# Performance work log

Measured on AMD Instinct MI355X. Metric: run time of the kernel, lower is better.

Reference implementation:

```python
import jax, jax.numpy as jnp
import numpy as np

N_NODES = 50000
N_EDGES = 800000
D = 128
BN_EPS = 1e-5


def setup_inputs() -> dict:
    key = jax.random.key(0)
    ks = jax.random.split(key, 8)
    scale = 1.0 / np.sqrt(D)
    return {
        "nfeat": jax.random.normal(ks[0], (N_NODES, D), dtype=jnp.float32),
        "efeat": jax.random.normal(ks[1], (N_EDGES, D), dtype=jnp.float32),
        "src": jax.random.randint(ks[2], (N_EDGES,), 0, N_NODES, dtype=jnp.int32),
        "dst": jax.random.randint(ks[3], (N_EDGES,), 0, N_NODES, dtype=jnp.int32),
        "W1": jax.random.normal(ks[4], (D, D), dtype=jnp.float32) * scale,
        "b1": jnp.zeros((D,), dtype=jnp.float32),
        "gamma": jnp.ones((D,), dtype=jnp.float32),
        "beta": jnp.zeros((D,), dtype=jnp.float32),
        "W2": jax.random.normal(ks[5], (D, D), dtype=jnp.float32) * scale,
        "b2": jnp.zeros((D,), dtype=jnp.float32),
        "We": jax.random.normal(ks[6], (D, D), dtype=jnp.float32) * scale,
        "be": jnp.zeros((D,), dtype=jnp.float32),
    }


def reference(nfeat, efeat, src, dst, W1, b1, gamma, beta, W2, b2, We, be):
    n = nfeat.shape[0]
    # GINConv, sum aggregator, eps=0: h = (1+eps)*x + sum_{j in N(i)} x_j
    agg = jax.ops.segment_sum(nfeat[src], dst, num_segments=n)  # [N, D]
    h = nfeat + agg
    # apply_func: Linear -> BatchNorm1d (training-mode batch stats) -> ReLU -> Linear
    h = h @ W1 + b1
    mu = jnp.mean(h, axis=0)
    var = jnp.mean(jnp.square(h - mu), axis=0)  # biased variance, as BatchNorm uses
    h = gamma * (h - mu) * jax.lax.rsqrt(var + BN_EPS) + beta
    h = jax.nn.relu(h)
    h = h @ W2 + b2
    # edge branch: linear on edge feats, scatter-sum to destination nodes, residual add
    e = efeat @ We + be                                          # [E, D]
    h_e = jax.ops.segment_sum(e, dst, num_segments=n)            # [N, D]
    return h + h_e
```

## Files before the change

### kernel.cpp

```cpp
#include <hip/hip_runtime.h>

#define D 128
#define TR 64
#define BK 32

static __device__ __forceinline__ float4 f4add(float4 a, float4 b) {
    return make_float4(a.x + b.x, a.y + b.y, a.z + b.z, a.w + b.w);
}


__global__ void k_hist(const int* __restrict__ dst, int* __restrict__ cnt, int E) {
    const int e = blockIdx.x * 256 + threadIdx.x;
    if (e < E) atomicAdd(&cnt[dst[e]], 1);
}

__global__ __launch_bounds__(256) void k_scan1(const int* __restrict__ cnt,
                                               int* __restrict__ row_ptr,
                                               int* __restrict__ bsum, int N) {
    __shared__ int sh[256];
    const int t = threadIdx.x;
    const int base = blockIdx.x * 1024 + t * 4;
    int4 v = make_int4(0, 0, 0, 0);
    if (base + 3 < N) v = *(const int4*)(cnt + base);
    else {
        if (base     < N) v.x = cnt[base];
        if (base + 1 < N) v.y = cnt[base + 1];
        if (base + 2 < N) v.z = cnt[base + 2];
        if (base + 3 < N) v.w = cnt[base + 3];
    }
    const int s = v.x + v.y + v.z + v.w;
    sh[t] = s;
    __syncthreads();
    for (int off = 1; off < 256; off <<= 1) {
        int tmp = (t >= off) ? sh[t - off] : 0;
        __syncthreads();
        sh[t] += tmp;
        __syncthreads();
    }
    const int p = sh[t] - s;
    if (base     < N) row_ptr[base]     = p;
    if (base + 1 < N) row_ptr[base + 1] = p + v.x;
    if (base + 2 < N) row_ptr[base + 2] = p + v.x + v.y;
    if (base + 3 < N) row_ptr[base + 3] = p + v.x + v.y + v.z;
    if (t == 255) bsum[blockIdx.x] = sh[255];
}

__global__ __launch_bounds__(256) void k_scan2(int* __restrict__ bsum, int nb) {
    __shared__ int sh[256];
    const int t = threadIdx.x;
    const int v = (t < nb) ? bsum[t] : 0;
    sh[t] = v;
    __syncthreads();
    for (int off = 1; off < 256; off <<= 1) {
        int tmp = (t >= off) ? sh[t - off] : 0;
        __syncthreads();
        sh[t] += tmp;
        __syncthreads();
    }
    if (t < nb) bsum[t] = sh[t] - v;
}

__global__ __launch_bounds__(256) void k_scan3(int* __restrict__ row_ptr,
                                               int* __restrict__ cursor,
                                               const int* __restrict__ bsum,
                                               int N, int E) {
    const int t = threadIdx.x;
    const int base = blockIdx.x * 1024 + t * 4;
    const int off = bsum[blockIdx.x];
    #pragma unroll
    for (int j = 0; j < 4; ++j) {
        const int i = base + j;
        if (i < N) {
            const int r = row_ptr[i] + off;
            row_ptr[i] = r;
            cursor[i] = r;
        }
    }
    if (blockIdx.x == 0 && t == 0) row_ptr[N] = E;
}

__global__ void k_scatter(const int* __restrict__ src, const int* __restrict__ dst,
                          int* __restrict__ cursor,
                          int* __restrict__ eidx, int* __restrict__ esrc, int E) {
    const int e = blockIdx.x * 256 + threadIdx.x;
    if (e < E) {
        const int d = dst[e];
        const int p = atomicAdd(&cursor[d], 1);
        eidx[p] = e;
        esrc[p] = src[e];
    }
}

__global__ __launch_bounds__(256) void k_gather(const float* __restrict__ nfeat,
                                                const float* __restrict__ efeat,
                                                const int* __restrict__ row_ptr,
                                                const int* __restrict__ eidx,
                                                const int* __restrict__ esrc,
                                                float* __restrict__ agg_n,
                                                float* __restrict__ agg_e,
                                                int N) {
    const int t = threadIdx.x;
    const int lane = t & 63;
    const int node = blockIdx.x * 4 + (t >> 6);
    if (node >= N) return;
    const float2* nf2 = (const float2*)nfeat;
    const float2* ef2 = (const float2*)efeat;
    const int start = row_ptr[node];
    const int end = row_ptr[node + 1];
    float2 an = make_float2(0.f, 0.f);
    float2 ae = make_float2(0.f, 0.f);
    int i = start;
    for (; i + 1 < end; i += 2) {
        const int e0 = eidx[i],     s0 = esrc[i];
        const int e1 = eidx[i + 1], s1 = esrc[i + 1];
        const float2 ev0 = ef2[(size_t)e0 * 64 + lane];
        const float2 nv0 = nf2[(size_t)s0 * 64 + lane];
        const float2 ev1 = ef2[(size_t)e1 * 64 + lane];
        const float2 nv1 = nf2[(size_t)s1 * 64 + lane];
        ae.x += ev0.x + ev1.x; ae.y += ev0.y + ev1.y;
        an.x += nv0.x + nv1.x; an.y += nv0.y + nv1.y;
    }
    if (i < end) {
        const int e0 = eidx[i], s0 = esrc[i];
        const float2 ev0 = ef2[(size_t)e0 * 64 + lane];
        const float2 nv0 = nf2[(size_t)s0 * 64 + lane];
        ae.x += ev0.x; ae.y += ev0.y;
        an.x += nv0.x; an.y += nv0.y;
    }
    ((float2*)agg_n)[(size_t)node * 64 + lane] = an;
    ((float2*)agg_e)[(size_t)node * 64 + lane] = ae;
}

#define FMA_ROW(i, xv)                                                         \
    acc[i][0] += xv * w0.x; acc[i][1] += xv * w0.y;                            \
    acc[i][2] += xv * w0.z; acc[i][3] += xv * w0.w;                            \
    acc[i][4] += xv * w1.x; acc[i][5] += xv * w1.y;                            \
    acc[i][6] += xv * w1.z; acc[i][7] += xv * w1.w;

__global__ __launch_bounds__(256) void k_h1(const float* __restrict__ nfeat,
                                            const float* __restrict__ agg_n,
                                            const float* __restrict__ W1,
                                            const float* __restrict__ b1,
                                            float* __restrict__ h1,
                                            float* __restrict__ stats,
                                            int N) {
    __shared__ float xs[TR * 132];
    __shared__ float wsh[BK * 128];
    const int t = threadIdx.x;
    const int row0 = blockIdx.x * TR;

    for (int i = t; i < TR * 32; i += 256) {
        const int r = i >> 5, c4 = i & 31;
        const int row = row0 + r;
        float4 v = make_float4(0.f, 0.f, 0.f, 0.f);
        if (row < N) {
            const float4 a = *(const float4*)(nfeat + row * D + c4 * 4);
            const float4 g = *(const float4*)(agg_n + row * D + c4 * 4);
            v = f4add(a, g);
        }
        *(float4*)(xs + r * 132 + c4 * 4) = v;
    }

    float acc[4][8];
    #pragma unroll
    for (int i = 0; i < 4; ++i)
        #pragma unroll
        for (int j = 0; j < 8; ++j) acc[i][j] = 0.f;

    const int rg = (t >> 4) * 4;
    const int c  = t & 15;

    for (int kc = 0; kc < D; kc += BK) {
        __syncthreads();
        #pragma unroll
        for (int i = 0; i < 4; ++i) {
            const int slot = i * 256 + t;
            const int k = slot >> 5, ch = slot & 31;
            *(float4*)(wsh + k * 128 + ch * 4) =
                *(const float4*)(W1 + (kc + k) * D + ch * 4);
        }
        __syncthreads();
        #pragma unroll 8
        for (int k = 0; k < BK; ++k) {
            const float4 w0 = *(const float4*)(wsh + k * 128 + c * 4);
            const float4 w1 = *(const float4*)(wsh + k * 128 + 64 + c * 4);
            const float x0 = xs[(rg + 0) * 132 + kc + k];
            const float x1 = xs[(rg + 1) * 132 + kc + k];
            const float x2 = xs[(rg + 2) * 132 + kc + k];
            const float x3 = xs[(rg + 3) * 132 + kc + k];
            FMA_ROW(0, x0)
            FMA_ROW(1, x1)
            FMA_ROW(2, x2)
            FMA_ROW(3, x3)
        }
    }

    const float4 bb0 = *(const float4*)(b1 + c * 4);
    const float4 bb1 = *(const float4*)(b1 + 64 + c * 4);
    float cs[8], cq[8];
    #pragma unroll
    for (int j = 0; j < 8; ++j) { cs[j] = 0.f; cq[j] = 0.f; }

    #pragma unroll
    for (int i = 0; i < 4; ++i) {
        const int row = row0 + rg + i;
        if (row < N) {
            float h[8];
            h[0] = acc[i][0] + bb0.x; h[1] = acc[i][1] + bb0.y;
            h[2] = acc[i][2] + bb0.z; h[3] = acc[i][3] + bb0.w;
            h[4] = acc[i][4] + bb1.x; h[5] = acc[i][5] + bb1.y;
            h[6] = acc[i][6] + bb1.z; h[7] = acc[i][7] + bb1.w;
            *(float4*)(h1 + row * D + c * 4)      = make_float4(h[0], h[1], h[2], h[3]);
            *(float4*)(h1 + row * D + 64 + c * 4) = make_float4(h[4], h[5], h[6], h[7]);
            #pragma unroll
            for (int j = 0; j < 8; ++j) { cs[j] += h[j]; cq[j] += h[j] * h[j]; }
        }
    }

    __syncthreads();
    float* red = wsh;
    const int g = t >> 4;
    #pragma unroll
    for (int j = 0; j < 4; ++j) {
        red[g * 256 +       4 * c + j] = cs[j];
        red[g * 256 +  64 + 4 * c + j] = cs[4 + j];
        red[g * 256 + 128 + 4 * c + j] = cq[j];
        red[g * 256 + 192 + 4 * c + j] = cq[4 + j];
    }
    __syncthreads();
    float v = 0.f;
    #pragma unroll
    for (int g2 = 0; g2 < 16; ++g2) v += red[g2 * 256 + t];
    atomicAdd(stats + t, v);
}

__global__ void k_bn_finalize(float* __restrict__ stats,
                              const float* __restrict__ gamma,
                              const float* __restrict__ beta,
                              int N) {
    const int c = threadIdx.x;
    const float invN = 1.0f / (float)N;
    const float sum = stats[c];
    const float sq  = stats[D + c];
    const float mu  = sum * invN;
    const float var = sq * invN - mu * mu;
    const float sc  = gamma[c] * rsqrtf(var + 1e-5f);
    const float sh  = beta[c] - mu * sc;
    stats[c]     = sc;
    stats[D + c] = sh;
}

__global__ __launch_bounds__(256) void k_out(const float* __restrict__ h1,
                                             const float* __restrict__ agg_e,
                                             const float* __restrict__ stats,
                                             const float* __restrict__ W2,
                                             const float* __restrict__ b2,
                                             const float* __restrict__ We,
                                             const float* __restrict__ be,
                                             const int* __restrict__ row_ptr,
                                             float* __restrict__ out,
                                             int N) {
    __shared__ float xs[TR * 132];
    __shared__ float wsh[BK * 128];
    const int t = threadIdx.x;
    const int row0 = blockIdx.x * TR;
    const int rg = (t >> 4) * 4;
    const int c  = t & 15;

    float acc[4][8];
    #pragma unroll
    for (int i = 0; i < 4; ++i)
        #pragma unroll
        for (int j = 0; j < 8; ++j) acc[i][j] = 0.f;

    for (int i = t; i < TR * 32; i += 256) {
        const int r = i >> 5, c4 = i & 31;
        const int row = row0 + r;
        float4 v = make_float4(0.f, 0.f, 0.f, 0.f);
        if (row < N) {
            const float4 h  = *(const float4*)(h1 + row * D + c4 * 4);
            const float4 sc = *(const float4*)(stats + c4 * 4);
            const float4 sh = *(const float4*)(stats + 128 + c4 * 4);
            v.x = fmaxf(h.x * sc.x + sh.x, 0.f);
            v.y = fmaxf(h.y * sc.y + sh.y, 0.f);
            v.z = fmaxf(h.z * sc.z + sh.z, 0.f);
            v.w = fmaxf(h.w * sc.w + sh.w, 0.f);
        }
        *(float4*)(xs + r * 132 + c4 * 4) = v;
    }
    for (int kc = 0; kc < D; kc += BK) {
        __syncthreads();
        #pragma unroll
        for (int i = 0; i < 4; ++i) {
            const int slot = i * 256 + t;
            const int k = slot >> 5, ch = slot & 31;
            *(float4*)(wsh + k * 128 + ch * 4) =
                *(const float4*)(W2 + (kc + k) * D + ch * 4);
        }
        __syncthreads();
        #pragma unroll 8
        for (int k = 0; k < BK; ++k) {
            const float4 w0 = *(const float4*)(wsh + k * 128 + c * 4);
            const float4 w1 = *(const float4*)(wsh + k * 128 + 64 + c * 4);
            const float x0 = xs[(rg + 0) * 132 + kc + k];
            const float x1 = xs[(rg + 1) * 132 + kc + k];
            const float x2 = xs[(rg + 2) * 132 + kc + k];
            const float x3 = xs[(rg + 3) * 132 + kc + k];
            FMA_ROW(0, x0)
            FMA_ROW(1, x1)
            FMA_ROW(2, x2)
            FMA_ROW(3, x3)
        }
    }
    __syncthreads();

    for (int i = t; i < TR * 32; i += 256) {
        const int r = i >> 5, c4 = i & 31;
        const int row = row0 + r;
        float4 v = make_float4(0.f, 0.f, 0.f, 0.f);
        if (row < N) v = *(const float4*)(agg_e + row * D + c4 * 4);
        *(float4*)(xs + r * 132 + c4 * 4) = v;
    }
    for (int kc = 0; kc < D; kc += BK) {
        __syncthreads();
        #pragma unroll
        for (int i = 0; i < 4; ++i) {
            const int slot = i * 256 + t;
            const int k = slot >> 5, ch = slot & 31;
            *(float4*)(wsh + k * 128 + ch * 4) =
                *(const float4*)(We + (kc + k) * D + ch * 4);
        }
        __syncthreads();
        #pragma unroll 8
        for (int k = 0; k < BK; ++k) {
            const float4 w0 = *(const float4*)(wsh + k * 128 + c * 4);
            const float4 w1 = *(const float4*)(wsh + k * 128 + 64 + c * 4);
            const float x0 = xs[(rg + 0) * 132 + kc + k];
            const float x1 = xs[(rg + 1) * 132 + kc + k];
            const float x2 = xs[(rg + 2) * 132 + kc + k];
            const float x3 = xs[(rg + 3) * 132 + kc + k];
            FMA_ROW(0, x0)
            FMA_ROW(1, x1)
            FMA_ROW(2, x2)
            FMA_ROW(3, x3)
        }
    }

    const float4 b20 = *(const float4*)(b2 + c * 4);
    const float4 b21 = *(const float4*)(b2 + 64 + c * 4);
    const float4 be0 = *(const float4*)(be + c * 4);
    const float4 be1 = *(const float4*)(be + 64 + c * 4);
    #pragma unroll
    for (int i = 0; i < 4; ++i) {
        const int row = row0 + rg + i;
        if (row < N) {
            const float dg = (float)(row_ptr[row + 1] - row_ptr[row]);
            const float4 o0 = make_float4(acc[i][0] + b20.x + dg * be0.x,
                                          acc[i][1] + b20.y + dg * be0.y,
                                          acc[i][2] + b20.z + dg * be0.z,
                                          acc[i][3] + b20.w + dg * be0.w);
            const float4 o1 = make_float4(acc[i][4] + b21.x + dg * be1.x,
                                          acc[i][5] + b21.y + dg * be1.y,
                                          acc[i][6] + b21.z + dg * be1.z,
                                          acc[i][7] + b21.w + dg * be1.w);
            *(float4*)(out + row * D + c * 4)      = o0;
            *(float4*)(out + row * D + 64 + c * 4) = o1;
        }
    }
}

extern "C" void kernel_launch(void* const* d_in, const int* in_sizes, int n_in,
                              void* d_out, int out_size, void* d_ws, size_t ws_size,
                              hipStream_t stream) {
    const float* nfeat = (const float*)d_in[0];
    const float* efeat = (const float*)d_in[1];
    const int*   src   = (const int*)d_in[2];
    const int*   dst   = (const int*)d_in[3];
    const float* W1    = (const float*)d_in[4];
    const float* b1    = (const float*)d_in[5];
    const float* gamma = (const float*)d_in[6];
    const float* beta  = (const float*)d_in[7];
    const float* W2    = (const float*)d_in[8];
    const float* b2    = (const float*)d_in[9];
    const float* We    = (const float*)d_in[10];
    const float* be    = (const float*)d_in[11];
    float* out = (float*)d_out;

    const int N = in_sizes[0] / D;
    const int E = in_sizes[2];

    float* ws      = (float*)d_ws;
    float* agg_n   = ws;
    float* h1      = agg_n;
    float* agg_e   = ws + (size_t)N * D;
    float* stats   = ws + (size_t)2 * N * D;
    int*   row_ptr = (int*)(stats + 256);
    int*   cursor  = row_ptr + (N + 16);
    int*   cnt     = cursor + (N + 16);
    int*   bsum    = cnt + (N + 16);
    int*   eidx    = bsum + 64;
    int*   esrc    = eidx + E;

    hipMemsetAsync(cnt, 0, (size_t)N * sizeof(int), stream);
    hipMemsetAsync(stats, 0, 256 * sizeof(float), stream);

    const int ebl = (E + 255) / 256;
    const int scb = (N + 1023) / 1024;

    k_hist<<<ebl, 256, 0, stream>>>(dst, cnt, E);
    k_scan1<<<scb, 256, 0, stream>>>(cnt, row_ptr, bsum, N);
    k_scan2<<<1, 256, 0, stream>>>(bsum, scb);
    k_scan3<<<scb, 256, 0, stream>>>(row_ptr, cursor, bsum, N, E);
    k_scatter<<<ebl, 256, 0, stream>>>(src, dst, cursor, eidx, esrc, E);

    k_gather<<<(N + 3) / 4, 256, 0, stream>>>(nfeat, efeat, row_ptr, eidx, esrc,
                                              agg_n, agg_e, N);

    const int nb = (N + TR - 1) / TR;
    k_h1<<<nb, 256, 0, stream>>>(nfeat, agg_n, W1, b1, h1, stats, N);
    k_bn_finalize<<<1, 128, 0, stream>>>(stats, gamma, beta, N);
    k_out<<<nb, 256, 0, stream>>>(h1, agg_e, stats, W2, b2, We, be, row_ptr, out, N);
}
```

Baseline: 345.8 us.

## Pack edge pairs, split wave across edges, fuse self-add into gather

The two memsets become a single zeroing kernel. The histogram and scatter kernels now handle four edges per thread through int4 loads of dst/src, and the scatter writes one interleaved int2 (edge index, source) per slot instead of two separate arrays. The gather kernel uses float4 loads with each half-wave taking alternate edges and combines the halves with a cross-lane shuffle; it also adds the node's own features, so k_h1 reads one buffer instead of two. These changes target launch overhead, index-load count and redundant feature reads, at the cost of extra shuffles and idle half-waves on low-degree nodes.

```diff
diff --git a/kernel.cpp b/kernel.cpp
--- a/kernel.cpp
+++ b/kernel.cpp
@@ -8,10 +8,23 @@
     return make_float4(a.x + b.x, a.y + b.y, a.z + b.z, a.w + b.w);
 }
 
+__global__ void k_zero(int* __restrict__ cnt, float* __restrict__ stats, int N) {
+    const int i = blockIdx.x * 256 + threadIdx.x;
+    if (i < N) cnt[i] = 0;
+    if (i < 256) stats[i] = 0.f;
+}
 
 __global__ void k_hist(const int* __restrict__ dst, int* __restrict__ cnt, int E) {
-    const int e = blockIdx.x * 256 + threadIdx.x;
-    if (e < E) atomicAdd(&cnt[dst[e]], 1);
+    const int base = (blockIdx.x * 256 + threadIdx.x) * 4;
+    if (base + 3 < E) {
+        const int4 d4 = *(const int4*)(dst + base);
+        atomicAdd(&cnt[d4.x], 1);
+        atomicAdd(&cnt[d4.y], 1);
+        atomicAdd(&cnt[d4.z], 1);
+        atomicAdd(&cnt[d4.w], 1);
+    } else {
+        for (int e = base; e < E; ++e) atomicAdd(&cnt[dst[e]], 1);
+    }
 }
 
 __global__ __launch_bounds__(256) void k_scan1(const int* __restrict__ cnt,
@@ -81,54 +94,65 @@
 
 __global__ void k_scatter(const int* __restrict__ src, const int* __restrict__ dst,
                           int* __restrict__ cursor,
-                          int* __restrict__ eidx, int* __restrict__ esrc, int E) {
-    const int e = blockIdx.x * 256 + threadIdx.x;
-    if (e < E) {
-        const int d = dst[e];
-        const int p = atomicAdd(&cursor[d], 1);
-        eidx[p] = e;
-        esrc[p] = src[e];
+                          int2* __restrict__ epair, int E) {
+    const int base = (blockIdx.x * 256 + threadIdx.x) * 4;
+    if (base + 3 < E) {
+        const int4 d4 = *(const int4*)(dst + base);
+        const int4 s4 = *(const int4*)(src + base);
+        int p;
+        p = atomicAdd(&cursor[d4.x], 1); epair[p] = make_int2(base + 0, s4.x);
+        p = atomicAdd(&cursor[d4.y], 1); epair[p] = make_int2(base + 1, s4.y);
+        p = atomicAdd(&cursor[d4.z], 1); epair[p] = make_int2(base + 2, s4.z);
+        p = atomicAdd(&cursor[d4.w], 1); epair[p] = make_int2(base + 3, s4.w);
+    } else {
+        for (int e = base; e < E; ++e) {
+            const int p = atomicAdd(&cursor[dst[e]], 1);
+            epair[p] = make_int2(e, src[e]);
+        }
     }
 }
 
 __global__ __launch_bounds__(256) void k_gather(const float* __restrict__ nfeat,
                                                 const float* __restrict__ efeat,
                                                 const int* __restrict__ row_ptr,
-                                                const int* __restrict__ eidx,
-                                                const int* __restrict__ esrc,
-                                                float* __restrict__ agg_n,
+                                                const int2* __restrict__ epair,
+                                                float* __restrict__ xbuf,
                                                 float* __restrict__ agg_e,
                                                 int N) {
     const int t = threadIdx.x;
     const int lane = t & 63;
+    const int h = lane >> 5;
+    const int c = lane & 31;
     const int node = blockIdx.x * 4 + (t >> 6);
     if (node >= N) return;
-    const float2* nf2 = (const float2*)nfeat;
-    const float2* ef2 = (const float2*)efeat;
+
     const int start = row_ptr[node];
-    const int end = row_ptr[node + 1];
-    float2 an = make_float2(0.f, 0.f);
-    float2 ae = make_float2(0.f, 0.f);
-    int i = start;
-    for (; i + 1 < end; i += 2) {
-        const int e0 = eidx[i],     s0 = esrc[i];
-        const int e1 = eidx[i + 1], s1 = esrc[i + 1];
-        const float2 ev0 = ef2[(size_t)e0 * 64 + lane];
-        const float2 nv0 = nf2[(size_t)s0 * 64 + lane];
-        const float2 ev1 = ef2[(size_t)e1 * 64 + lane];
-        const float2 nv1 = nf2[(size_t)s1 * 64 + lane];
-        ae.x += ev0.x + ev1.x; ae.y += ev0.y + ev1.y;
-        an.x += nv0.x + nv1.x; an.y += nv0.y + nv1.y;
-    }
-    if (i < end) {
-        const int e0 = eidx[i], s0 = esrc[i];
-        const float2 ev0 = ef2[(size_t)e0 * 64 + lane];
-        const float2 nv0 = nf2[(size_t)s0 * 64 + lane];
-        ae.x += ev0.x; ae.y += ev0.y;
-        an.x += nv0.x; an.y += nv0.y;
-    }
-    ((float2*)agg_n)[(size_t)node * 64 + lane] = an;
-    ((float2*)agg_e)[(size_t)node * 64 + lane] = ae;
+    const int end   = row_ptr[node + 1];
+
+    float4 an = make_float4(0.f, 0.f, 0.f, 0.f);
+    float4 ae = make_float4(0.f, 0.f, 0.f, 0.f);
+    for (int e = start + h; e < end; e += 2) {
+        const int2 p = epair[e];
+        const float4 ev = *(const float4*)(efeat + (size_t)p.x * D + c * 4);
+        const float4 nv = *(const float4*)(nfeat + (size_t)p.y * D + c * 4);
+        ae = f4add(ae, ev);
+        an = f4add(an, nv);
+    }
+    float4 an_t, ae_t;
+    an_t.x = an.x + __shfl_xor(an.x, 32);
+    an_t.y = an.y + __shfl_xor(an.y, 32);
+    an_t.z = an.z + __shfl_xor(an.z, 32);
+    an_t.w = an.w + __shfl_xor(an.w, 32);
+    ae_t.x = ae.x + __shfl_xor(ae.x, 32);
+    ae_t.y = ae.y + __shfl_xor(ae.y, 32);
+    ae_t.z = ae.z + __shfl_xor(ae.z, 32);
+    ae_t.w = ae.w + __shfl_xor(ae.w, 32);
+
+    if (h == 0) {
+        const float4 self = *(const float4*)(nfeat + (size_t)node * D + c * 4);
+        *(float4*)(xbuf  + (size_t)node * D + c * 4) = f4add(self, an_t);
+        *(float4*)(agg_e + (size_t)node * D + c * 4) = ae_t;
+    }
 }
 
 #define FMA_ROW(i, xv)                                                         \
@@ -137,8 +161,7 @@
     acc[i][4] += xv * w1.x; acc[i][5] += xv * w1.y;                            \
     acc[i][6] += xv * w1.z; acc[i][7] += xv * w1.w;
 
-__global__ __launch_bounds__(256) void k_h1(const float* __restrict__ nfeat,
-                                            const float* __restrict__ agg_n,
+__global__ __launch_bounds__(256) void k_h1(const float* __restrict__ xbuf,
                                             const float* __restrict__ W1,
                                             const float* __restrict__ b1,
                                             float* __restrict__ h1,
@@ -153,11 +176,7 @@
         const int r = i >> 5, c4 = i & 31;
         const int row = row0 + r;
         float4 v = make_float4(0.f, 0.f, 0.f, 0.f);
-        if (row < N) {
-            const float4 a = *(const float4*)(nfeat + row * D + c4 * 4);
-            const float4 g = *(const float4*)(agg_n + row * D + c4 * 4);
-            v = f4add(a, g);
-        }
+        if (row < N) v = *(const float4*)(xbuf + (size_t)row * D + c4 * 4);
         *(float4*)(xs + r * 132 + c4 * 4) = v;
     }
 
@@ -210,8 +229,8 @@
             h[2] = acc[i][2] + bb0.z; h[3] = acc[i][3] + bb0.w;
             h[4] = acc[i][4] + bb1.x; h[5] = acc[i][5] + bb1.y;
             h[6] = acc[i][6] + bb1.z; h[7] = acc[i][7] + bb1.w;
-            *(float4*)(h1 + row * D + c * 4)      = make_float4(h[0], h[1], h[2], h[3]);
-            *(float4*)(h1 + row * D + 64 + c * 4) = make_float4(h[4], h[5], h[6], h[7]);
+            *(float4*)(h1 + (size_t)row * D + c * 4)      = make_float4(h[0], h[1], h[2], h[3]);
+            *(float4*)(h1 + (size_t)row * D + 64 + c * 4) = make_float4(h[4], h[5], h[6], h[7]);
             #pragma unroll
             for (int j = 0; j < 8; ++j) { cs[j] += h[j]; cq[j] += h[j] * h[j]; }
         }
@@ -278,7 +297,7 @@
         const int row = row0 + r;
         float4 v = make_float4(0.f, 0.f, 0.f, 0.f);
         if (row < N) {
-            const float4 h  = *(const float4*)(h1 + row * D + c4 * 4);
+            const float4 h  = *(const float4*)(h1 + (size_t)row * D + c4 * 4);
             const float4 sc = *(const float4*)(stats + c4 * 4);
             const float4 sh = *(const float4*)(stats + 128 + c4 * 4);
             v.x = fmaxf(h.x * sc.x + sh.x, 0.f);
@@ -318,7 +337,7 @@
         const int r = i >> 5, c4 = i & 31;
         const int row = row0 + r;
         float4 v = make_float4(0.f, 0.f, 0.f, 0.f);
-        if (row < N) v = *(const float4*)(agg_e + row * D + c4 * 4);
+        if (row < N) v = *(const float4*)(agg_e + (size_t)row * D + c4 * 4);
         *(float4*)(xs + r * 132 + c4 * 4) = v;
     }
     for (int kc = 0; kc < D; kc += BK) {
@@ -363,8 +382,8 @@
                                           acc[i][5] + b21.y + dg * be1.y,
                                           acc[i][6] + b21.z + dg * be1.z,
                                           acc[i][7] + b21.w + dg * be1.w);
-            *(float4*)(out + row * D + c * 4)      = o0;
-            *(float4*)(out + row * D + 64 + c * 4) = o1;
+            *(float4*)(out + (size_t)row * D + c * 4)      = o0;
+            *(float4*)(out + (size_t)row * D + 64 + c * 4) = o1;
         }
     }
 }
@@ -390,34 +409,31 @@
     const int E = in_sizes[2];
 
     float* ws      = (float*)d_ws;
-    float* agg_n   = ws;
-    float* h1      = agg_n;
+    float* xbuf    = ws;
+    float* h1      = xbuf;
     float* agg_e   = ws + (size_t)N * D;
     float* stats   = ws + (size_t)2 * N * D;
     int*   row_ptr = (int*)(stats + 256);
     int*   cursor  = row_ptr + (N + 16);
     int*   cnt     = cursor + (N + 16);
     int*   bsum    = cnt + (N + 16);
-    int*   eidx    = bsum + 64;
-    int*   esrc    = eidx + E;
-
-    hipMemsetAsync(cnt, 0, (size_t)N * sizeof(int), stream);
-    hipMemsetAsync(stats, 0, 256 * sizeof(float), stream);
-
-    const int ebl = (E + 255) / 256;
-    const int scb = (N + 1023) / 1024;
-
-    k_hist<<<ebl, 256, 0, stream>>>(dst, cnt, E);
+    int2*  epair   = (int2*)(bsum + 64);
+
+    const int ebl4 = (E / 4 + 255) / 256;
+    const int scb  = (N + 1023) / 1024;
+
+    k_zero<<<(N + 255) / 256, 256, 0, stream>>>(cnt, stats, N);
+    k_hist<<<ebl4, 256, 0, stream>>>(dst, cnt, E);
     k_scan1<<<scb, 256, 0, stream>>>(cnt, row_ptr, bsum, N);
     k_scan2<<<1, 256, 0, stream>>>(bsum, scb);
     k_scan3<<<scb, 256, 0, stream>>>(row_ptr, cursor, bsum, N, E);
-    k_scatter<<<ebl, 256, 0, stream>>>(src, dst, cursor, eidx, esrc, E);
-
-    k_gather<<<(N + 3) / 4, 256, 0, stream>>>(nfeat, efeat, row_ptr, eidx, esrc,
-                                              agg_n, agg_e, N);
+    k_scatter<<<ebl4, 256, 0, stream>>>(src, dst, cursor, epair, E);
+
+    k_gather<<<(N + 3) / 4, 256, 0, stream>>>(nfeat, efeat, row_ptr, epair,
+                                              xbuf, agg_e, N);
 
     const int nb = (N + TR - 1) / TR;
-    k_h1<<<nb, 256, 0, stream>>>(nfeat, agg_n, W1, b1, h1, stats, N);
+    k_h1<<<nb, 256, 0, stream>>>(xbuf, W1, b1, h1, stats, N);
     k_bn_finalize<<<1, 128, 0, stream>>>(stats, gamma, beta, N);
     k_out<<<nb, 256, 0, stream>>>(h1, agg_e, stats, W2, b2, We, be, row_ptr, out, N);
 }
```

After: 333.7 us. 3.5% less time.
